# Kernel optimization log

Hardware: AMD Instinct MI355X
Metric: run time of the kernel (lower is better)

## Reference

```python
import jax, jax.numpy as jnp
import numpy as np

B, T, C, H = 2, 2048, 1024, 16
HD = C // H  # head dim = 64


def setup_inputs() -> dict:
    key = jax.random.key(0)
    ks = jax.random.split(key, 5)
    s = 1.0 / np.sqrt(C)
    return {
        "x": jax.random.normal(ks[0], (B, T, C), dtype=jnp.float32),
        "Wq": jax.random.normal(ks[1], (C, C), dtype=jnp.float32) * s,
        "bq": jnp.zeros((C,), dtype=jnp.float32),
        "Wk": jax.random.normal(ks[2], (C, C), dtype=jnp.float32) * s,
        "bk": jnp.zeros((C,), dtype=jnp.float32),
        "Wv": jax.random.normal(ks[3], (C, C), dtype=jnp.float32) * s,
        "bv": jnp.zeros((C,), dtype=jnp.float32),
        "Wp": jax.random.normal(ks[4], (C, C), dtype=jnp.float32) * s,
        "bp": jnp.zeros((C,), dtype=jnp.float32),
    }


def reference(x, Wq, bq, Wk, bk, Wv, bv, Wp, bp):
    # QKV projections -> [B, H, T, HD]
    def proj(W, b):
        return (x @ W.T + b).reshape(B, T, H, HD).transpose(0, 2, 1, 3)

    q = proj(Wq, bq)
    k = proj(Wk, bk)
    v = proj(Wv, bv)

    scale = 1.0 / np.sqrt(HD)
    att = jnp.einsum("bhtd,bhsd->bhts", q, k) * scale  # [B,H,T,T]
    causal = jnp.tril(jnp.ones((T, T), dtype=bool))
    att = jnp.where(causal, att, -jnp.inf)
    att = jax.nn.softmax(att, axis=-1)
    y = jnp.einsum("bhts,bhsd->bhtd", att, v)          # [B,H,T,HD]
    y = y.transpose(0, 2, 1, 3).reshape(B, T, C)
    return y @ Wp.T + bp
```

## Files before the change

### kernel.cpp

```cpp
#include <hip/hip_runtime.h>
#include <hip/hip_bf16.h>

#define BB 2
#define TT 2048
#define CC 1024
#define HH 16
#define HDD 64

typedef __attribute__((ext_vector_type(8))) short bf16x8;
typedef __attribute__((ext_vector_type(4))) float f32x4;

static __device__ __forceinline__ unsigned short f2bf(float f) {
  union { float f; unsigned u; } v; v.f = f;
  unsigned r = v.u + 0x7fffu + ((v.u >> 16) & 1u);
  return (unsigned short)(r >> 16);
}

static __device__ __forceinline__ unsigned fbits(float f) {
  union { float f; unsigned u; } v; v.f = f; return v.u;
}

static __device__ __forceinline__ unsigned pk_trunc(float lo, float hi) {
  return __builtin_amdgcn_perm(fbits(hi), fbits(lo), 0x07060302u);
}

static __device__ __forceinline__ void gload_lds16(const unsigned short* g, unsigned short* l) {
  __builtin_amdgcn_global_load_lds((const __attribute__((address_space(1))) void*)g,
                                   (__attribute__((address_space(3))) void*)l, 16, 0, 0);
}

__global__ __launch_bounds__(256) void convert_all(
    const float* __restrict__ x, const float* __restrict__ Wq,
    const float* __restrict__ Wk, const float* __restrict__ Wv,
    const float* __restrict__ Wp, unsigned short* __restrict__ dst)
{
  const size_t M4 = 4194304, M1 = 1048576;
  const size_t e = ((size_t)blockIdx.x * 256 + threadIdx.x) * 8;
  const float* src; size_t off;
  if (e < M4)            { src = x;  off = e; }
  else if (e < M4 + M1)  { src = Wq; off = e - M4; }
  else if (e < M4 + 2*M1){ src = Wk; off = e - M4 - M1; }
  else if (e < M4 + 3*M1){ src = Wv; off = e - M4 - 2*M1; }
  else                   { src = Wp; off = e - M4 - 3*M1; }
  float4 a = *(const float4*)(src + off);
  float4 c = *(const float4*)(src + off + 4);
  unsigned short buf[8] = {f2bf(a.x), f2bf(a.y), f2bf(a.z), f2bf(a.w),
                           f2bf(c.x), f2bf(c.y), f2bf(c.z), f2bf(c.w)};
  *(uint4*)(dst + e) = *(const uint4*)buf;
}

__global__ __launch_bounds__(256) void gemm_mfma(
    const unsigned short* __restrict__ A, const unsigned short* __restrict__ W,
    const float* __restrict__ b0, const float* __restrict__ b1, const float* __restrict__ b2,
    unsigned short* __restrict__ oQ, unsigned short* __restrict__ oK,
    unsigned short* __restrict__ oVt)
{
  __shared__ unsigned short As[128][32];
  __shared__ unsigned short Bs[128][32];
  const int t = threadIdx.x;
  const int wv = __builtin_amdgcn_readfirstlane(t >> 6);
  const int ln = t & 63;
  const int l16 = ln & 15;
  const int quad = ln >> 4;
  const int mBase = blockIdx.x * 128;
  const int nBase = blockIdx.y * 128;
  const int wm = (wv >> 1) * 64, wn = (wv & 1) * 64;

  f32x4 acc[4][4];
#pragma unroll
  for (int i = 0; i < 4; i++)
#pragma unroll
    for (int j = 0; j < 4; j++) acc[i][j] = (f32x4){0.f, 0.f, 0.f, 0.f};

  const int ca = wv * 64 + ln;
  const int cb = ca + 256;
  const int ra = ca >> 2, colA = (ca & 3) * 8;
  const int rb = cb >> 2, colB = (cb & 3) * 8;
  unsigned short* ldsA0 = &As[0][0] + (size_t)(wv * 64) * 8;
  unsigned short* ldsA1 = &As[0][0] + (size_t)(256 + wv * 64) * 8;
  unsigned short* ldsB0 = &Bs[0][0] + (size_t)(wv * 64) * 8;
  unsigned short* ldsB1 = &Bs[0][0] + (size_t)(256 + wv * 64) * 8;
  const unsigned short* apA0 = A + (size_t)(mBase + ra) * CC + colA;
  const unsigned short* apA1 = A + (size_t)(mBase + rb) * CC + colB;
  const unsigned short* apB0 = W + (size_t)(nBase + ra) * CC + colA;
  const unsigned short* apB1 = W + (size_t)(nBase + rb) * CC + colB;

  for (int kb = 0; kb < CC; kb += 32) {
    __syncthreads();
    gload_lds16(apA0 + kb, ldsA0);
    gload_lds16(apA1 + kb, ldsA1);
    gload_lds16(apB0 + kb, ldsB0);
    gload_lds16(apB1 + kb, ldsB1);
    __syncthreads();
    bf16x8 af[4], bfr[4];
#pragma unroll
    for (int i = 0; i < 4; i++) af[i] = *(const bf16x8*)&As[wm + i * 16 + l16][quad * 8];
#pragma unroll
    for (int j = 0; j < 4; j++) bfr[j] = *(const bf16x8*)&Bs[wn + j * 16 + l16][quad * 8];
#pragma unroll
    for (int i = 0; i < 4; i++)
#pragma unroll
      for (int j = 0; j < 4; j++)
        acc[i][j] = __builtin_amdgcn_mfma_f32_16x16x32_bf16(af[i], bfr[j], acc[i][j], 0, 0, 0);
  }

  const int which = nBase >> 10;
  const float* bias = which == 0 ? b0 : (which == 1 ? b1 : b2);
  unsigned short* dst = which == 0 ? oQ : (which == 1 ? oK : oVt);
  const float scl = which == 0 ? 0.1803368801f : 1.0f;
#pragma unroll
  for (int i = 0; i < 4; i++)
#pragma unroll
    for (int r = 0; r < 4; r++) {
      const int m = mBase + wm + i * 16 + quad * 4 + r;
      const int b = m >> 11, tp = m & 2047;
#pragma unroll
      for (int j = 0; j < 4; j++) {
        const int n = nBase + wn + j * 16 + l16;
        const int nl = n & 1023, h = nl >> 6, d = nl & 63;
        const unsigned short v = f2bf((acc[i][j][r] + bias[nl]) * scl);
        if (which < 2) dst[((size_t)(b * HH + h) * TT + tp) * HDD + d] = v;
        else           dst[((size_t)(b * HH + h) * HDD + d) * TT + tp] = v;
      }
    }
}

__global__ __launch_bounds__(256) void gemm_proj(
    const unsigned short* __restrict__ A, const unsigned short* __restrict__ W,
    const float* __restrict__ bias, float* __restrict__ out)
{
  __shared__ unsigned short As[64][32];
  __shared__ unsigned short Bs[64][32];
  const int t = threadIdx.x;
  const int wv = __builtin_amdgcn_readfirstlane(t >> 6);
  const int ln = t & 63;
  const int l16 = ln & 15;
  const int quad = ln >> 4;
  const int mBase = blockIdx.x * 64;
  const int nBase = blockIdx.y * 64;
  const int wm = (wv >> 1) * 32, wn = (wv & 1) * 32;

  f32x4 acc[2][2];
#pragma unroll
  for (int i = 0; i < 2; i++)
#pragma unroll
    for (int j = 0; j < 2; j++) acc[i][j] = (f32x4){0.f, 0.f, 0.f, 0.f};

  const int rs = t >> 2, cs = (t & 3) * 8;
  unsigned short* ldsA = &As[0][0] + (size_t)t * 8;
  unsigned short* ldsB = &Bs[0][0] + (size_t)t * 8;
  const unsigned short* apA = A + (size_t)(mBase + rs) * CC + cs;
  const unsigned short* apB = W + (size_t)(nBase + rs) * CC + cs;

  for (int kb = 0; kb < CC; kb += 32) {
    __syncthreads();
    gload_lds16(apA + kb, ldsA);
    gload_lds16(apB + kb, ldsB);
    __syncthreads();
    bf16x8 af[2], bfr[2];
#pragma unroll
    for (int i = 0; i < 2; i++) af[i] = *(const bf16x8*)&As[wm + i * 16 + l16][quad * 8];
#pragma unroll
    for (int j = 0; j < 2; j++) bfr[j] = *(const bf16x8*)&Bs[wn + j * 16 + l16][quad * 8];
#pragma unroll
    for (int i = 0; i < 2; i++)
#pragma unroll
      for (int j = 0; j < 2; j++)
        acc[i][j] = __builtin_amdgcn_mfma_f32_16x16x32_bf16(af[i], bfr[j], acc[i][j], 0, 0, 0);
  }

#pragma unroll
  for (int i = 0; i < 2; i++)
#pragma unroll
    for (int r = 0; r < 4; r++) {
      const int m = mBase + wm + i * 16 + quad * 4 + r;
#pragma unroll
      for (int j = 0; j < 2; j++) {
        const int n = nBase + wn + j * 16 + l16;
        out[(size_t)m * CC + n] = acc[i][j][r] + bias[n];
      }
    }
}

__global__ __launch_bounds__(256, 2) void attn_mfma(
    const unsigned short* __restrict__ Q, const unsigned short* __restrict__ K,
    const unsigned short* __restrict__ Vt, unsigned short* __restrict__ y)
{
  __shared__ unsigned short QP[128][72];
  __shared__ unsigned short Ks[2][64][72];
  __shared__ unsigned short Vts[2][64][72];

  const int t = threadIdx.x;
  const int a = blockIdx.x;
  const int bh = blockIdx.y;
  const int wave = t >> 6;
  const int lane = t & 63;
  const int l16 = lane & 15;
  const int quad = lane >> 4;

  const size_t base = (size_t)bh * TT * HDD;
  const int qtL = a, qtH = 31 - a;
  const int qBaseL = qtL * 64, qBaseH = qtH * 64;

#pragma unroll
  for (int p = 0; p < 4; p++) {
    const int c = p * 256 + t;
    const int r = c >> 3, off = (c & 7) * 8;
    const int srcRow = (r < 64) ? (qBaseL + r) : (qBaseH + r - 64);
    *(uint4*)&QP[r][off] = *(const uint4*)(Q + base + (size_t)srcRow * HDD + off);
  }

  const int sr = t >> 2, sc = (t & 3) * 8;
  const unsigned short* kbase = K + base + (size_t)sr * HDD + sc;
  const unsigned short* vbase = Vt + base + (size_t)sr * TT + sc;
  uint4 kr0 = *(const uint4*)(kbase);
  uint4 kr1 = *(const uint4*)(kbase + 32);
  uint4 vr0 = *(const uint4*)(vbase);
  uint4 vr1 = *(const uint4*)(vbase + 32);
  __syncthreads();

  bf16x8 qfL0 = *(const bf16x8*)&QP[wave * 16 + l16][quad * 8];
  bf16x8 qfL1 = *(const bf16x8*)&QP[wave * 16 + l16][32 + quad * 8];
  bf16x8 qfH0 = *(const bf16x8*)&QP[64 + wave * 16 + l16][quad * 8];
  bf16x8 qfH1 = *(const bf16x8*)&QP[64 + wave * 16 + l16][32 + quad * 8];
  unsigned short (*PtH)[72] = (unsigned short (*)[72])&QP[wave * 16];
  unsigned short (*PtL)[72] = (unsigned short (*)[72])&QP[64 + wave * 16];

  float lL = 0.f, lH = 0.f;
  f32x4 OfrL[4], OfrH[4];
#pragma unroll
  for (int dt = 0; dt < 4; dt++) {
    OfrL[dt] = (f32x4){0.f, 0.f, 0.f, 0.f};
    OfrH[dt] = (f32x4){0.f, 0.f, 0.f, 0.f};
  }

  for (int kt = 0; kt <= qtH; kt++) {
    const int buf = kt & 1;
    *(uint4*)&Ks[buf][sr][sc]       = kr0;
    *(uint4*)&Ks[buf][sr][sc + 32]  = kr1;
    *(uint4*)&Vts[buf][sr][sc]      = vr0;
    *(uint4*)&Vts[buf][sr][sc + 32] = vr1;
    __syncthreads();
    if (kt < qtH) {
      kr0 = *(const uint4*)(kbase + (size_t)(kt + 1) * 64 * HDD);
      kr1 = *(const uint4*)(kbase + (size_t)(kt + 1) * 64 * HDD + 32);
      vr0 = *(const uint4*)(vbase + (kt + 1) * 64);
      vr1 = *(const uint4*)(vbase + (kt + 1) * 64 + 32);
    }
    const bool doLo = (kt <= qtL);

    f32x4 StH[4], StL[4];
#pragma unroll
    for (int ct = 0; ct < 4; ct++) {
      bf16x8 a0 = *(const bf16x8*)&Ks[buf][ct * 16 + l16][quad * 8];
      bf16x8 a1 = *(const bf16x8*)&Ks[buf][ct * 16 + l16][32 + quad * 8];
      f32x4 s = (f32x4){0.f, 0.f, 0.f, 0.f};
      s = __builtin_amdgcn_mfma_f32_16x16x32_bf16(a0, qfH0, s, 0, 0, 0);
      s = __builtin_amdgcn_mfma_f32_16x16x32_bf16(a1, qfH1, s, 0, 0, 0);
      StH[ct] = s;
      if (doLo) {
        f32x4 s2 = (f32x4){0.f, 0.f, 0.f, 0.f};
        s2 = __builtin_amdgcn_mfma_f32_16x16x32_bf16(a0, qfL0, s2, 0, 0, 0);
        s2 = __builtin_amdgcn_mfma_f32_16x16x32_bf16(a1, qfL1, s2, 0, 0, 0);
        StL[ct] = s2;
      }
    }

    if (kt == qtH) {
#pragma unroll
      for (int ct = 0; ct < 4; ct++) {
        float p[4];
#pragma unroll
        for (int r = 0; r < 4; r++) {
          float pv = exp2f(StH[ct][r]);
          if (ct * 16 + quad * 4 + r > wave * 16 + l16) pv = 0.f;
          lH += pv;
          p[r] = pv;
        }
        uint2 pk = {pk_trunc(p[0], p[1]), pk_trunc(p[2], p[3])};
        *(uint2*)&PtH[l16][ct * 16 + quad * 4] = pk;
      }
    } else {
#pragma unroll
      for (int ct = 0; ct < 4; ct++) {
        float p[4];
#pragma unroll
        for (int r = 0; r < 4; r++) {
          const float pv = exp2f(StH[ct][r]);
          lH += pv;
          p[r] = pv;
        }
        uint2 pk = {pk_trunc(p[0], p[1]), pk_trunc(p[2], p[3])};
        *(uint2*)&PtH[l16][ct * 16 + quad * 4] = pk;
      }
    }
    if (doLo) {
      if (kt == qtL) {
#pragma unroll
        for (int ct = 0; ct < 4; ct++) {
          float p[4];
#pragma unroll
          for (int r = 0; r < 4; r++) {
            float pv = exp2f(StL[ct][r]);
            if (ct * 16 + quad * 4 + r > wave * 16 + l16) pv = 0.f;
            lL += pv;
            p[r] = pv;
          }
          uint2 pk = {pk_trunc(p[0], p[1]), pk_trunc(p[2], p[3])};
          *(uint2*)&PtL[l16][ct * 16 + quad * 4] = pk;
        }
      } else {
#pragma unroll
        for (int ct = 0; ct < 4; ct++) {
          float p[4];
#pragma unroll
          for (int r = 0; r < 4; r++) {
            const float pv = exp2f(StL[ct][r]);
            lL += pv;
            p[r] = pv;
          }
          uint2 pk = {pk_trunc(p[0], p[1]), pk_trunc(p[2], p[3])};
          *(uint2*)&PtL[l16][ct * 16 + quad * 4] = pk;
        }
      }
    }

    bf16x8 paH0 = *(const bf16x8*)&PtH[l16][quad * 8];
    bf16x8 paH1 = *(const bf16x8*)&PtH[l16][32 + quad * 8];
    bf16x8 paL0, paL1;
    if (doLo) {
      paL0 = *(const bf16x8*)&PtL[l16][quad * 8];
      paL1 = *(const bf16x8*)&PtL[l16][32 + quad * 8];
    }
#pragma unroll
    for (int dt = 0; dt < 4; dt++) {
      bf16x8 vb0 = *(const bf16x8*)&Vts[buf][dt * 16 + l16][quad * 8];
      bf16x8 vb1 = *(const bf16x8*)&Vts[buf][dt * 16 + l16][32 + quad * 8];
      OfrH[dt] = __builtin_amdgcn_mfma_f32_16x16x32_bf16(paH0, vb0, OfrH[dt], 0, 0, 0);
      OfrH[dt] = __builtin_amdgcn_mfma_f32_16x16x32_bf16(paH1, vb1, OfrH[dt], 0, 0, 0);
      if (doLo) {
        OfrL[dt] = __builtin_amdgcn_mfma_f32_16x16x32_bf16(paL0, vb0, OfrL[dt], 0, 0, 0);
        OfrL[dt] = __builtin_amdgcn_mfma_f32_16x16x32_bf16(paL1, vb1, OfrL[dt], 0, 0, 0);
      }
    }
  }

  lL += __shfl_xor(lL, 16, 64); lL += __shfl_xor(lL, 32, 64);
  lH += __shfl_xor(lH, 16, 64); lH += __shfl_xor(lH, 32, 64);

  const int b = bh >> 4, h = bh & 15;
  float lRowL[4], lRowH[4];
#pragma unroll
  for (int r = 0; r < 4; r++) {
    lRowL[r] = __shfl(lL, quad * 4 + r, 16);
    lRowH[r] = __shfl(lH, quad * 4 + r, 16);
  }
#pragma unroll
  for (int r = 0; r < 4; r++) {
    const int qL = qBaseL + wave * 16 + quad * 4 + r;
    const int qH = qBaseH + wave * 16 + quad * 4 + r;
    const float invL = 1.0f / lRowL[r];
    const float invH = 1.0f / lRowH[r];
    unsigned short* ypL = y + ((size_t)(b * TT + qL)) * CC + h * 64 + l16;
    unsigned short* ypH = y + ((size_t)(b * TT + qH)) * CC + h * 64 + l16;
#pragma unroll
    for (int dt = 0; dt < 4; dt++) {
      ypL[dt * 16] = f2bf(OfrL[dt][r] * invL);
      ypH[dt * 16] = f2bf(OfrH[dt][r] * invH);
    }
  }
}

extern "C" void kernel_launch(void* const* d_in, const int* in_sizes, int n_in,
                              void* d_out, int out_size, void* d_ws, size_t ws_size,
                              hipStream_t stream) {
  const float* x  = (const float*)d_in[0];
  const float* Wq = (const float*)d_in[1];
  const float* bq = (const float*)d_in[2];
  const float* Wk = (const float*)d_in[3];
  const float* bk = (const float*)d_in[4];
  const float* Wv = (const float*)d_in[5];
  const float* bv = (const float*)d_in[6];
  const float* Wp = (const float*)d_in[7];
  const float* bp = (const float*)d_in[8];

  const size_t M4 = 4194304, M1 = 1048576;
  unsigned short* xb   = (unsigned short*)d_ws;
  unsigned short* wqb  = xb + M4;
  unsigned short* wpb  = wqb + 3 * M1;
  unsigned short* wsQ  = wpb + M1;
  unsigned short* wsK  = wsQ + M4;
  unsigned short* wsVt = wsK + M4;
  unsigned short* yb   = wsVt + M4;

  convert_all<<<4096, 256, 0, stream>>>(x, Wq, Wk, Wv, Wp, xb);
  gemm_mfma<<<dim3(32, 24), 256, 0, stream>>>(xb, wqb, bq, bk, bv,
                                              wsQ, wsK, wsVt);
  attn_mfma<<<dim3(16, BB * HH), 256, 0, stream>>>(wsQ, wsK, wsVt, yb);
  gemm_proj<<<dim3(64, 16), 256, 0, stream>>>(yb, wpb, bp, (float*)d_out);
}
```

Measured before the change: 187.8 us.

## Load K/V fragments directly from global into registers; enlarge proj GEMM M tile

The attention kernel drops its LDS double-buffered K and V tiles. Each wave now loads its MFMA operand fragments for K and V^T straight from global memory into registers, prefetching the next tile after each use. This removes the per-iteration __syncthreads and the LDS store/load traffic, at the cost of every wave redundantly reading the same K/V data from global/L2 and holding more live registers. Separately, the output projection GEMM moves to 128x64 tiles with 2-block occupancy, halving its grid and improving A/B reuse per block.

```diff
diff --git a/kernel.cpp b/kernel.cpp
--- a/kernel.cpp
+++ b/kernel.cpp
@@ -125,52 +125,58 @@
     }
 }
 
-__global__ __launch_bounds__(256) void gemm_proj(
+__global__ __launch_bounds__(256, 2) void gemm_proj(
     const unsigned short* __restrict__ A, const unsigned short* __restrict__ W,
     const float* __restrict__ bias, float* __restrict__ out)
 {
-  __shared__ unsigned short As[64][32];
+  __shared__ unsigned short As[128][32];
   __shared__ unsigned short Bs[64][32];
   const int t = threadIdx.x;
   const int wv = __builtin_amdgcn_readfirstlane(t >> 6);
   const int ln = t & 63;
   const int l16 = ln & 15;
   const int quad = ln >> 4;
-  const int mBase = blockIdx.x * 64;
+  const int mBase = blockIdx.x * 128;
   const int nBase = blockIdx.y * 64;
-  const int wm = (wv >> 1) * 32, wn = (wv & 1) * 32;
-
-  f32x4 acc[2][2];
-#pragma unroll
-  for (int i = 0; i < 2; i++)
+  const int wm = (wv >> 1) * 64, wn = (wv & 1) * 32;
+
+  f32x4 acc[4][2];
+#pragma unroll
+  for (int i = 0; i < 4; i++)
 #pragma unroll
     for (int j = 0; j < 2; j++) acc[i][j] = (f32x4){0.f, 0.f, 0.f, 0.f};
 
-  const int rs = t >> 2, cs = (t & 3) * 8;
-  unsigned short* ldsA = &As[0][0] + (size_t)t * 8;
-  unsigned short* ldsB = &Bs[0][0] + (size_t)t * 8;
-  const unsigned short* apA = A + (size_t)(mBase + rs) * CC + cs;
-  const unsigned short* apB = W + (size_t)(nBase + rs) * CC + cs;
+  const int ca = wv * 64 + ln;
+  const int cb = ca + 256;
+  const int ra = ca >> 2, colA = (ca & 3) * 8;
+  const int rb = cb >> 2, colB = (cb & 3) * 8;
+  unsigned short* ldsA0 = &As[0][0] + (size_t)(wv * 64) * 8;
+  unsigned short* ldsA1 = &As[0][0] + (size_t)(256 + wv * 64) * 8;
+  unsigned short* ldsB0 = &Bs[0][0] + (size_t)(wv * 64) * 8;
+  const unsigned short* apA0 = A + (size_t)(mBase + ra) * CC + colA;
+  const unsigned short* apA1 = A + (size_t)(mBase + rb) * CC + colB;
+  const unsigned short* apB0 = W + (size_t)(nBase + ra) * CC + colA;
 
   for (int kb = 0; kb < CC; kb += 32) {
     __syncthreads();
-    gload_lds16(apA + kb, ldsA);
-    gload_lds16(apB + kb, ldsB);
+    gload_lds16(apA0 + kb, ldsA0);
+    gload_lds16(apA1 + kb, ldsA1);
+    gload_lds16(apB0 + kb, ldsB0);
     __syncthreads();
-    bf16x8 af[2], bfr[2];
-#pragma unroll
-    for (int i = 0; i < 2; i++) af[i] = *(const bf16x8*)&As[wm + i * 16 + l16][quad * 8];
+    bf16x8 af[4], bfr[2];
+#pragma unroll
+    for (int i = 0; i < 4; i++) af[i] = *(const bf16x8*)&As[wm + i * 16 + l16][quad * 8];
 #pragma unroll
     for (int j = 0; j < 2; j++) bfr[j] = *(const bf16x8*)&Bs[wn + j * 16 + l16][quad * 8];
 #pragma unroll
-    for (int i = 0; i < 2; i++)
+    for (int i = 0; i < 4; i++)
 #pragma unroll
       for (int j = 0; j < 2; j++)
         acc[i][j] = __builtin_amdgcn_mfma_f32_16x16x32_bf16(af[i], bfr[j], acc[i][j], 0, 0, 0);
   }
 
 #pragma unroll
-  for (int i = 0; i < 2; i++)
+  for (int i = 0; i < 4; i++)
 #pragma unroll
     for (int r = 0; r < 4; r++) {
       const int m = mBase + wm + i * 16 + quad * 4 + r;
@@ -187,8 +193,6 @@
     const unsigned short* __restrict__ Vt, unsigned short* __restrict__ y)
 {
   __shared__ unsigned short QP[128][72];
-  __shared__ unsigned short Ks[2][64][72];
-  __shared__ unsigned short Vts[2][64][72];
 
   const int t = threadIdx.x;
   const int a = blockIdx.x;
@@ -210,13 +214,20 @@
     *(uint4*)&QP[r][off] = *(const uint4*)(Q + base + (size_t)srcRow * HDD + off);
   }
 
-  const int sr = t >> 2, sc = (t & 3) * 8;
-  const unsigned short* kbase = K + base + (size_t)sr * HDD + sc;
-  const unsigned short* vbase = Vt + base + (size_t)sr * TT + sc;
-  uint4 kr0 = *(const uint4*)(kbase);
-  uint4 kr1 = *(const uint4*)(kbase + 32);
-  uint4 vr0 = *(const uint4*)(vbase);
-  uint4 vr1 = *(const uint4*)(vbase + 32);
+  const unsigned short* kRow = K  + base + l16 * HDD + quad * 8;
+  const unsigned short* vRow = Vt + base + (size_t)l16 * TT + quad * 8;
+
+  bf16x8 kc[4][2], vc[4][2];
+#pragma unroll
+  for (int ct = 0; ct < 4; ct++) {
+    kc[ct][0] = *(const bf16x8*)(kRow + ct * (16 * HDD));
+    kc[ct][1] = *(const bf16x8*)(kRow + ct * (16 * HDD) + 32);
+  }
+#pragma unroll
+  for (int dt = 0; dt < 4; dt++) {
+    vc[dt][0] = *(const bf16x8*)(vRow + (size_t)dt * (16 * TT));
+    vc[dt][1] = *(const bf16x8*)(vRow + (size_t)dt * (16 * TT) + 32);
+  }
   __syncthreads();
 
   bf16x8 qfL0 = *(const bf16x8*)&QP[wave * 16 + l16][quad * 8];
@@ -235,34 +246,29 @@
   }
 
   for (int kt = 0; kt <= qtH; kt++) {
-    const int buf = kt & 1;
-    *(uint4*)&Ks[buf][sr][sc]       = kr0;
-    *(uint4*)&Ks[buf][sr][sc + 32]  = kr1;
-    *(uint4*)&Vts[buf][sr][sc]      = vr0;
-    *(uint4*)&Vts[buf][sr][sc + 32] = vr1;
-    __syncthreads();
-    if (kt < qtH) {
-      kr0 = *(const uint4*)(kbase + (size_t)(kt + 1) * 64 * HDD);
-      kr1 = *(const uint4*)(kbase + (size_t)(kt + 1) * 64 * HDD + 32);
-      vr0 = *(const uint4*)(vbase + (kt + 1) * 64);
-      vr1 = *(const uint4*)(vbase + (kt + 1) * 64 + 32);
-    }
     const bool doLo = (kt <= qtL);
 
     f32x4 StH[4], StL[4];
 #pragma unroll
     for (int ct = 0; ct < 4; ct++) {
-      bf16x8 a0 = *(const bf16x8*)&Ks[buf][ct * 16 + l16][quad * 8];
-      bf16x8 a1 = *(const bf16x8*)&Ks[buf][ct * 16 + l16][32 + quad * 8];
       f32x4 s = (f32x4){0.f, 0.f, 0.f, 0.f};
-      s = __builtin_amdgcn_mfma_f32_16x16x32_bf16(a0, qfH0, s, 0, 0, 0);
-      s = __builtin_amdgcn_mfma_f32_16x16x32_bf16(a1, qfH1, s, 0, 0, 0);
+      s = __builtin_amdgcn_mfma_f32_16x16x32_bf16(kc[ct][0], qfH0, s, 0, 0, 0);
+      s = __builtin_amdgcn_mfma_f32_16x16x32_bf16(kc[ct][1], qfH1, s, 0, 0, 0);
       StH[ct] = s;
       if (doLo) {
         f32x4 s2 = (f32x4){0.f, 0.f, 0.f, 0.f};
-        s2 = __builtin_amdgcn_mfma_f32_16x16x32_bf16(a0, qfL0, s2, 0, 0, 0);
-        s2 = __builtin_amdgcn_mfma_f32_16x16x32_bf16(a1, qfL1, s2, 0, 0, 0);
+        s2 = __builtin_amdgcn_mfma_f32_16x16x32_bf16(kc[ct][0], qfL0, s2, 0, 0, 0);
+        s2 = __builtin_amdgcn_mfma_f32_16x16x32_bf16(kc[ct][1], qfL1, s2, 0, 0, 0);
         StL[ct] = s2;
+      }
+    }
+
+    if (kt < qtH) {
+      const unsigned short* kp = kRow + (size_t)(kt + 1) * (64 * HDD);
+#pragma unroll
+      for (int ct = 0; ct < 4; ct++) {
+        kc[ct][0] = *(const bf16x8*)(kp + ct * (16 * HDD));
+        kc[ct][1] = *(const bf16x8*)(kp + ct * (16 * HDD) + 32);
       }
     }
 
@@ -334,13 +340,20 @@
     }
 #pragma unroll
     for (int dt = 0; dt < 4; dt++) {
-      bf16x8 vb0 = *(const bf16x8*)&Vts[buf][dt * 16 + l16][quad * 8];
-      bf16x8 vb1 = *(const bf16x8*)&Vts[buf][dt * 16 + l16][32 + quad * 8];
-      OfrH[dt] = __builtin_amdgcn_mfma_f32_16x16x32_bf16(paH0, vb0, OfrH[dt], 0, 0, 0);
-      OfrH[dt] = __builtin_amdgcn_mfma_f32_16x16x32_bf16(paH1, vb1, OfrH[dt], 0, 0, 0);
+      OfrH[dt] = __builtin_amdgcn_mfma_f32_16x16x32_bf16(paH0, vc[dt][0], OfrH[dt], 0, 0, 0);
+      OfrH[dt] = __builtin_amdgcn_mfma_f32_16x16x32_bf16(paH1, vc[dt][1], OfrH[dt], 0, 0, 0);
       if (doLo) {
-        OfrL[dt] = __builtin_amdgcn_mfma_f32_16x16x32_bf16(paL0, vb0, OfrL[dt], 0, 0, 0);
-        OfrL[dt] = __builtin_amdgcn_mfma_f32_16x16x32_bf16(paL1, vb1, OfrL[dt], 0, 0, 0);
+        OfrL[dt] = __builtin_amdgcn_mfma_f32_16x16x32_bf16(paL0, vc[dt][0], OfrL[dt], 0, 0, 0);
+        OfrL[dt] = __builtin_amdgcn_mfma_f32_16x16x32_bf16(paL1, vc[dt][1], OfrL[dt], 0, 0, 0);
+      }
+    }
+
+    if (kt < qtH) {
+      const unsigned short* vp = vRow + (kt + 1) * 64;
+#pragma unroll
+      for (int dt = 0; dt < 4; dt++) {
+        vc[dt][0] = *(const bf16x8*)(vp + (size_t)dt * (16 * TT));
+        vc[dt][1] = *(const bf16x8*)(vp + (size_t)dt * (16 * TT) + 32);
       }
     }
   }
@@ -397,5 +410,5 @@
   gemm_mfma<<<dim3(32, 24), 256, 0, stream>>>(xb, wqb, bq, bk, bv,
                                               wsQ, wsK, wsVt);
   attn_mfma<<<dim3(16, BB * HH), 256, 0, stream>>>(wsQ, wsK, wsVt, yb);
-  gemm_proj<<<dim3(64, 16), 256, 0, stream>>>(yb, wpb, bp, (float*)d_out);
-}
+  gemm_proj<<<dim3(32, 16), 256, 0, stream>>>(yb, wpb, bp, (float*)d_out);
+}
```

Measured after the change: 260.6 us. 38.8% more time.
